# Kernel tuning notes

Hardware: AMD Instinct MI355X
Metric: run time of the kernel (lower is better)

Reference implementation:

```python
import jax, jax.numpy as jnp
import numpy as np

N = 20000
E = 640000
D = 128
NORM_FACTOR = 100.0
LN_EPS = 1e-5


def _layer_norm(x, g, b):
    mu = jnp.mean(x, axis=-1, keepdims=True)
    var = jnp.var(x, axis=-1, keepdims=True)
    return (x - mu) * jax.lax.rsqrt(var + LN_EPS) * g + b


def setup_inputs() -> dict:
    key = jax.random.key(0)
    ks = jax.random.split(key, 16)

    def lin(k, fan_in, shape):
        bound = 1.0 / np.sqrt(fan_in)
        return jax.random.uniform(k, shape, jnp.float32, -bound, bound)

    h = jax.random.normal(ks[0], (N, D), jnp.float32)
    distances = jax.random.uniform(ks[1], (E, 1), jnp.float32)
    edges = jax.random.randint(ks[2], (2, E), 0, N, jnp.int64)
    node_mask = jnp.ones((N, 1), jnp.float32)
    edge_mask = jnp.ones((E, 1), jnp.float32)

    return {
        "h": h, "distances": distances, "node_mask": node_mask, "edge_mask": edge_mask,
        # linear: in->out
        "lin_w": lin(ks[3], D, (D, D)), "lin_b": lin(ks[4], D, (D,)),
        # att_mlp: (2D+1)->2D -> 2D->D -> D->1
        "att_w1": lin(ks[5], 2 * D + 1, (2 * D, 2 * D + 1)), "att_b1": lin(ks[5], 2 * D + 1, (2 * D,)),
        "att_w2": lin(ks[6], 2 * D, (D, 2 * D)), "att_b2": lin(ks[6], 2 * D, (D,)),
        "att_w3": lin(ks[7], D, (1, D)), "att_b3": lin(ks[7], D, (1,)),
        # node_mlp: D->D, LN, SiLU, D->D
        "nm_w1": lin(ks[8], D, (D, D)), "nm_b1": lin(ks[8], D, (D,)),
        "nm_ln_g": jnp.ones((D,), jnp.float32), "nm_ln_b": jnp.zeros((D,), jnp.float32),
        "nm_w2": lin(ks[9], D, (D, D)), "nm_b2": lin(ks[9], D, (D,)),
        # final LayerNorm
        "ln_g": jnp.ones((D,), jnp.float32), "ln_b": jnp.zeros((D,), jnp.float32),
        "edges": edges,
    }


def reference(h, distances, node_mask, edge_mask,
              lin_w, lin_b, att_w1, att_b1, att_w2, att_b2, att_w3, att_b3,
              nm_w1, nm_b1, nm_ln_g, nm_ln_b, nm_w2, nm_b2, ln_g, ln_b, edges):
    x = h @ lin_w.T + lin_b                                  # [N, D]
    row, col = edges[0], edges[1]
    x_row = x[row]                                           # [E, D]
    x_col = x[col]                                           # [E, D]

    # DenseAtt
    d = distances * edge_mask
    x_cat = jnp.concatenate([x_row, x_col, d], axis=1)       # [E, 2D+1]
    a = jax.nn.silu(x_cat @ att_w1.T + att_b1)
    a = jax.nn.silu(a @ att_w2.T + att_b2)
    att = jax.nn.sigmoid(a @ att_w3.T + att_b3) * edge_mask  # [E, 1]

    agg = x_col * att                                        # [E, D]
    out = jax.ops.segment_sum(agg, row, num_segments=N) / NORM_FACTOR

    # node_mlp + residual
    o = out @ nm_w1.T + nm_b1
    o = jax.nn.silu(_layer_norm(o, nm_ln_g, nm_ln_b))
    o = o @ nm_w2.T + nm_b2
    hh = o + x

    hh = _layer_norm(hh, ln_g, ln_b)
    hh = jax.nn.silu(hh)                                     # act = SiLU
    return hh
```

## Files before the change

### kernel.cpp

```cpp
#include <hip/hip_runtime.h>
#include <hip/hip_bf16.h>

#define N_NODES 20000
#define E_EDGES 640000
#define DIM 128
#define CAP 96
#define EPB 64
#define NPB 8
#define XST 264

typedef __attribute__((ext_vector_type(8))) short bf16x8;
typedef __attribute__((ext_vector_type(4))) float f32x4;
typedef __attribute__((ext_vector_type(2))) float f32x2;
typedef __attribute__((ext_vector_type(4))) unsigned u32x4;

#define LOG2E 1.44269504f
__device__ __forceinline__ float fsilu(float x) {
    return x * __builtin_amdgcn_rcpf(1.f + __builtin_amdgcn_exp2f(-LOG2E * x));
}
__device__ __forceinline__ float fsig(float x) {
    return __builtin_amdgcn_rcpf(1.f + __builtin_amdgcn_exp2f(-LOG2E * x));
}
__device__ __forceinline__ f32x2 fsilu2(f32x2 v) {
    f32x2 m = v * (-LOG2E);
    f32x2 e; e.x = __builtin_amdgcn_exp2f(m.x); e.y = __builtin_amdgcn_exp2f(m.y);
    f32x2 den = e + 1.0f;
    f32x2 r; r.x = __builtin_amdgcn_rcpf(den.x); r.y = __builtin_amdgcn_rcpf(den.y);
    return v * r;
}

__device__ __forceinline__ unsigned short f2bf(float x) {
    union { float f; unsigned u; } v; v.f = x;
    unsigned r = (v.u + 0x7fffu + ((v.u >> 16) & 1u)) >> 16;
    return (unsigned short)r;
}
__device__ __forceinline__ float bf2f(unsigned short s) {
    union { unsigned u; float f; } v; v.u = ((unsigned)s) << 16;
    return v.f;
}
__device__ __forceinline__ unsigned pack_bf16(float lo, float hi) {
    union { float f; unsigned u; } a, b; a.f = lo; b.f = hi;
    unsigned ul = a.u + 0x8000u, uh = b.u + 0x8000u;
    return __builtin_amdgcn_perm(uh, ul, 0x07060302u);
}

#define PRE_PREP_BLOCKS 64
#define PRE_LIN_BLOCKS  625
#define PRE_ADJ_BLOCKS  2500
__global__ __launch_bounds__(256) void pre_kernel(
    const float* __restrict__ w1, const float* __restrict__ w2,
    unsigned short* __restrict__ w1b, float* __restrict__ w1p,
    unsigned short* __restrict__ w2b,
    const float* __restrict__ h, const float* __restrict__ lw,
    const float* __restrict__ lb, float* __restrict__ x,
    unsigned short* __restrict__ xb,
    const int* __restrict__ edges, int* __restrict__ cnt,
    int2* __restrict__ adj2, int E) {
    __shared__ float hs[32][128];
    int b = blockIdx.x;
    int t = threadIdx.x;

    if (b < PRE_PREP_BLOCKS) {
        int i = b * 256 + t;
        const int stride = PRE_PREP_BLOCKS * 256;
        for (int idx = i; idx < 256 * 256; idx += stride) {
            int o = idx >> 8, k = idx & 255;
            w1b[idx] = f2bf(w1[o * 257 + k]);
        }
        for (int idx = i; idx < 128 * 256; idx += stride) {
            int n2 = idx >> 8, p = idx & 255;
            int bb = p & ~31, off = p & 31;
            int ksrc = bb + (off >> 1) + ((off & 1) << 4);
            w2b[idx] = f2bf(w2[n2 * 256 + ksrc]);
        }
        for (int idx = i; idx < 256; idx += stride) {
            int bb = idx & ~31, off = idx & 31;
            int ksrc = bb + (off >> 1) + ((off & 1) << 4);
            w1p[idx] = w1[ksrc * 257 + 256];
        }
    } else if (b < PRE_PREP_BLOCKS + PRE_LIN_BLOCKS) {
        int nb = b - PRE_PREP_BLOCKS;
        int n0 = nb * 32;
        int ch = t & 127, g = t >> 7;
#pragma unroll
        for (int j = 0; j < 16; ++j) hs[g * 16 + j][ch] = h[(size_t)(n0 + g * 16 + j) * DIM + ch];
        __syncthreads();
        float acc[16];
#pragma unroll
        for (int j = 0; j < 16; ++j) acc[j] = 0.f;
        for (int kc = 0; kc < 128; kc += 4) {
            float4 wv = *(const float4*)&lw[(size_t)ch * DIM + kc];
#pragma unroll
            for (int j = 0; j < 16; ++j) {
                float4 hv = *(const float4*)&hs[g * 16 + j][kc];
                acc[j] += wv.x * hv.x + wv.y * hv.y + wv.z * hv.z + wv.w * hv.w;
            }
        }
        float bias = lb[ch];
#pragma unroll
        for (int j = 0; j < 16; ++j) {
            float v = acc[j] + bias;
            int n = n0 + g * 16 + j;
            x[(size_t)n * DIM + ch] = v;
            xb[(size_t)n * DIM + ch] = f2bf(v);
        }
    } else {
        int e = (b - PRE_PREP_BLOCKS - PRE_LIN_BLOCKS) * 256 + t;
        if (e < E) {
            int r = edges[e];
            int col = edges[E + e];
            int slot = atomicAdd(&cnt[r], 1);
            if (slot < CAP) { int2 v; v.x = e; v.y = col; adj2[(size_t)r * CAP + slot] = v; }
        }
    }
}

#define PRC_NPB 16
__global__ __launch_bounds__(256) void prc_kernel(
    const unsigned short* __restrict__ xb,
    const unsigned short* __restrict__ w1b,
    const float* __restrict__ b1,
    unsigned short* __restrict__ prb, unsigned short* __restrict__ pcb) {
    int n0 = blockIdx.x * PRC_NPB;
    int w = threadIdx.x >> 6, lane = threadIdx.x & 63;
    int lrow = lane & 15, quad = lane >> 4;

    bf16x8 a[4];
#pragma unroll
    for (int kk = 0; kk < 4; ++kk)
        a[kk] = *(const bf16x8*)&xb[(size_t)(n0 + lrow) * DIM + kk * 32 + quad * 8];

    f32x4 z = {0.f, 0.f, 0.f, 0.f};
#pragma unroll
    for (int i = 0; i < 8; ++i) {
        int gt = w * 8 + i;
        int half = gt >> 4;
        int obase = (gt & 15) * 16;
        f32x4 acc = z;
#pragma unroll
        for (int kk = 0; kk < 4; ++kk) {
            bf16x8 bfrag = *(const bf16x8*)&w1b[(size_t)(obase + lrow) * 256 + half * 128 + kk * 32 + quad * 8];
            acc = __builtin_amdgcn_mfma_f32_16x16x32_bf16(a[kk], bfrag, acc, 0, 0, 0);
        }
        int o = obase + lrow;
        if (half == 0) {
            float bias = b1[o];
#pragma unroll
            for (int r = 0; r < 4; ++r)
                prb[(size_t)(n0 + quad * 4 + r) * 256 + o] = f2bf(acc[r] + bias);
        } else {
#pragma unroll
            for (int r = 0; r < 4; ++r)
                pcb[(size_t)(n0 + quad * 4 + r) * 256 + o] = f2bf(acc[r]);
        }
    }
}

__global__ __launch_bounds__(512, 4) void edge_kernel(
    const unsigned short* __restrict__ prb, const unsigned short* __restrict__ pcb,
    const float* __restrict__ dist, const float* __restrict__ emask,
    const int* __restrict__ edges,
    const float* __restrict__ w1p,
    const unsigned short* __restrict__ w2b, const float* __restrict__ b2,
    const float* __restrict__ w3, const float* __restrict__ b3v,
    float* __restrict__ attv, int E) {
    __shared__ unsigned short buf[EPB * XST];
    __shared__ float part[8][EPB];
    __shared__ float w1ps[256];

    int tid = threadIdx.x;
    int eb = blockIdx.x * EPB;

    if (tid < 256) w1ps[tid] = w1p[tid];

    int ge = tid >> 3, cb = tid & 7;
    int e = eb + ge;
    int r = edges[e];
    int c2 = edges[E + e];
    float d = dist[e] * emask[e];
    const unsigned short* prow = prb + (size_t)r * 256 + cb * 32;
    const unsigned short* pcp  = pcb + (size_t)c2 * 256 + cb * 32;

    bf16x8 pA0 = *(const bf16x8*)&prow[0];
    bf16x8 pB0 = *(const bf16x8*)&prow[16];
    bf16x8 qA0 = *(const bf16x8*)&pcp[0];
    bf16x8 qB0 = *(const bf16x8*)&pcp[16];
    bf16x8 pA1 = *(const bf16x8*)&prow[8];
    bf16x8 pB1 = *(const bf16x8*)&prow[24];
    bf16x8 qA1 = *(const bf16x8*)&pcp[8];
    bf16x8 qB1 = *(const bf16x8*)&pcp[24];

    int wave = tid >> 6, lane = tid & 63;
    int lrow = lane & 15, quad = lane >> 4;
    int n2 = wave * 16 + lrow;
    float bias2 = b2[n2];
    float w3v = w3[n2];

    __syncthreads();

    {
        const float* wp = &w1ps[cb * 32];
        f32x2 d2 = {d, d};
        unsigned u[16];
#pragma unroll
        for (int l = 0; l < 8; ++l) {
            f32x2 p = {bf2f((unsigned short)pA0[l]), bf2f((unsigned short)pB0[l])};
            f32x2 q = {bf2f((unsigned short)qA0[l]), bf2f((unsigned short)qB0[l])};
            f32x2 wv2 = *(const f32x2*)&wp[2 * l];
            f32x2 sv = fsilu2(p + q + d2 * wv2);
            u[l] = pack_bf16(sv.x, sv.y);
        }
#pragma unroll
        for (int l = 0; l < 8; ++l) {
            f32x2 p = {bf2f((unsigned short)pA1[l]), bf2f((unsigned short)pB1[l])};
            f32x2 q = {bf2f((unsigned short)qA1[l]), bf2f((unsigned short)qB1[l])};
            f32x2 wv2 = *(const f32x2*)&wp[16 + 2 * l];
            f32x2 sv = fsilu2(p + q + d2 * wv2);
            u[8 + l] = pack_bf16(sv.x, sv.y);
        }
        u32x4* w4 = (u32x4*)&buf[ge * XST + cb * 32];
        u32x4 v0 = {u[0], u[1], u[2], u[3]};
        u32x4 v1 = {u[4], u[5], u[6], u[7]};
        u32x4 v2 = {u[8], u[9], u[10], u[11]};
        u32x4 v3 = {u[12], u[13], u[14], u[15]};
        w4[0] = v0; w4[1] = v1; w4[2] = v2; w4[3] = v3;
    }
    __syncthreads();

    f32x4 zz = {0.f, 0.f, 0.f, 0.f};
    f32x4 acc2[4];
#pragma unroll
    for (int mt = 0; mt < 4; ++mt) acc2[mt] = zz;

    for (int kk = 0; kk < 8; ++kk) {
        int ka = kk * 32 + quad * 8;
        bf16x8 bfrag = *(const bf16x8*)&w2b[(size_t)n2 * 256 + ka];
#pragma unroll
        for (int mt = 0; mt < 4; ++mt) {
            bf16x8 a = *(bf16x8*)&buf[(mt * 16 + lrow) * XST + ka];
            acc2[mt] = __builtin_amdgcn_mfma_f32_16x16x32_bf16(a, bfrag, acc2[mt], 0, 0, 0);
        }
    }

    float s[4][4];
#pragma unroll
    for (int mt = 0; mt < 4; ++mt)
#pragma unroll
        for (int r2 = 0; r2 < 4; ++r2)
            s[mt][r2] = fsilu(acc2[mt][r2] + bias2) * w3v;
#pragma unroll
    for (int off2 = 1; off2 < 16; off2 <<= 1) {
#pragma unroll
        for (int mt = 0; mt < 4; ++mt)
#pragma unroll
            for (int r2 = 0; r2 < 4; ++r2)
                s[mt][r2] += __shfl_xor(s[mt][r2], off2);
    }
    if (lrow == 0) {
#pragma unroll
        for (int mt = 0; mt < 4; ++mt)
#pragma unroll
            for (int r2 = 0; r2 < 4; ++r2)
                part[wave][mt * 16 + quad * 4 + r2] = s[mt][r2];
    }
    __syncthreads();

    if (tid < EPB) {
        float ssum = b3v[0];
#pragma unroll
        for (int w = 0; w < 8; ++w) ssum += part[w][tid];
        attv[eb + tid] = fsig(ssum) * emask[eb + tid];
    }
}

__global__ __launch_bounds__(256) void node_kernel(
    const float* __restrict__ attv, const int2* __restrict__ adj2,
    const int* __restrict__ cnt,
    const unsigned short* __restrict__ xb,
    const float* __restrict__ x,
    const float* __restrict__ w1, const float* __restrict__ bb1,
    const float* __restrict__ lng, const float* __restrict__ lnb,
    const float* __restrict__ w2, const float* __restrict__ bb2,
    const float* __restrict__ gF, const float* __restrict__ bF,
    float* __restrict__ out, int E) {
    __shared__ float atts[NPB][CAP];
    __shared__ int   cols[NPB][CAP];
    __shared__ float outv[NPB][128];
    __shared__ float bufs[NPB][128];
    __shared__ float mu_s[NPB], rs_s[NPB];
    __shared__ int cnts[NPB];

    int t = threadIdx.x;
    int n0 = blockIdx.x * NPB;

    if (t < NPB) { int c = cnt[n0 + t]; cnts[t] = c > CAP ? CAP : c; }
    __syncthreads();

    {
        int jg = t >> 5, l = t & 31;
        int c = cnts[jg];
        const int2* al = adj2 + (size_t)(n0 + jg) * CAP;
        for (int i = l; i < c; i += 32) {
            int2 v = al[i];
            atts[jg][i] = attv[v.x];
            cols[jg][i] = v.y;
        }
    }
    __syncthreads();

    int w = t >> 6, lane = t & 63;
    int islot = lane >> 4;
    int co = lane & 15;
#pragma unroll
    for (int jj = 0; jj < 2; ++jj) {
        int j = w * 2 + jj;
        int c = cnts[j];
        float acc[8];
#pragma unroll
        for (int k = 0; k < 8; ++k) acc[k] = 0.f;
        for (int base = 0; base < c; base += 8) {
            int i0 = base + islot, i1 = base + 4 + islot;
            bool k0 = i0 < c, k1 = i1 < c;
            int c0 = cols[j][k0 ? i0 : 0];
            int c1 = cols[j][k1 ? i1 : 0];
            float a0 = k0 ? atts[j][i0] : 0.f;
            float a1 = k1 ? atts[j][i1] : 0.f;
            bf16x8 q0 = *(const bf16x8*)&xb[(size_t)c0 * DIM + co * 8];
            bf16x8 q1 = *(const bf16x8*)&xb[(size_t)c1 * DIM + co * 8];
#pragma unroll
            for (int k = 0; k < 8; ++k) acc[k] += a0 * bf2f((unsigned short)q0[k]);
#pragma unroll
            for (int k = 0; k < 8; ++k) acc[k] += a1 * bf2f((unsigned short)q1[k]);
        }
#pragma unroll
        for (int k = 0; k < 8; ++k) {
            acc[k] += __shfl_xor(acc[k], 16);
            acc[k] += __shfl_xor(acc[k], 32);
        }
        if (islot == 0) {
            float4 v0 = {acc[0] * 0.01f, acc[1] * 0.01f, acc[2] * 0.01f, acc[3] * 0.01f};
            float4 v1 = {acc[4] * 0.01f, acc[5] * 0.01f, acc[6] * 0.01f, acc[7] * 0.01f};
            *(float4*)&outv[j][co * 8] = v0;
            *(float4*)&outv[j][co * 8 + 4] = v1;
        }
    }
    __syncthreads();

    int h = t >> 7, ch = t & 127;
    float xres[4];
#pragma unroll
    for (int jj = 0; jj < 4; ++jj)
        xres[jj] = x[(size_t)(n0 + h * 4 + jj) * DIM + ch];

    float a1[4] = {0, 0, 0, 0};
    for (int kc = 0; kc < 128; kc += 4) {
        float4 wv = *(const float4*)&w1[(size_t)ch * DIM + kc];
#pragma unroll
        for (int jj = 0; jj < 4; ++jj) {
            int j = h * 4 + jj;
            float4 ov = *(const float4*)&outv[j][kc];
            a1[jj] += wv.x * ov.x + wv.y * ov.y + wv.z * ov.z + wv.w * ov.w;
        }
    }
    float bias1 = bb1[ch];
#pragma unroll
    for (int jj = 0; jj < 4; ++jj) bufs[h * 4 + jj][ch] = a1[jj] + bias1;
    __syncthreads();

    {
        int j = t >> 5, l = t & 31;
        float s = 0.f, qq = 0.f;
#pragma unroll
        for (int i = 0; i < 4; ++i) { float v = bufs[j][l + 32 * i]; s += v; qq += v * v; }
#pragma unroll
        for (int off2 = 16; off2; off2 >>= 1) { s += __shfl_xor(s, off2); qq += __shfl_xor(qq, off2); }
        if (l == 0) {
            float mu = s * (1.f / 128.f);
            float var = qq * (1.f / 128.f) - mu * mu;
            mu_s[j] = mu; rs_s[j] = __builtin_amdgcn_rsqf(var + 1e-5f);
        }
    }
    __syncthreads();

    float g = lng[ch], bb = lnb[ch];
    float h2[4];
#pragma unroll
    for (int jj = 0; jj < 4; ++jj) {
        int j = h * 4 + jj;
        h2[jj] = fsilu((bufs[j][ch] - mu_s[j]) * rs_s[j] * g + bb);
    }
    __syncthreads();
#pragma unroll
    for (int jj = 0; jj < 4; ++jj) bufs[h * 4 + jj][ch] = h2[jj];
    __syncthreads();

    float a3[4] = {0, 0, 0, 0};
    for (int kc = 0; kc < 128; kc += 4) {
        float4 wv = *(const float4*)&w2[(size_t)ch * DIM + kc];
#pragma unroll
        for (int jj = 0; jj < 4; ++jj) {
            int j = h * 4 + jj;
            float4 bv = *(const float4*)&bufs[j][kc];
            a3[jj] += wv.x * bv.x + wv.y * bv.y + wv.z * bv.z + wv.w * bv.w;
        }
    }
    float bias2 = bb2[ch];
    float hh[4];
#pragma unroll
    for (int jj = 0; jj < 4; ++jj) hh[jj] = a3[jj] + bias2 + xres[jj];
    __syncthreads();
#pragma unroll
    for (int jj = 0; jj < 4; ++jj) bufs[h * 4 + jj][ch] = hh[jj];
    __syncthreads();

    {
        int j = t >> 5, l = t & 31;
        float s = 0.f, qq = 0.f;
#pragma unroll
        for (int i = 0; i < 4; ++i) { float v = bufs[j][l + 32 * i]; s += v; qq += v * v; }
#pragma unroll
        for (int off2 = 16; off2; off2 >>= 1) { s += __shfl_xor(s, off2); qq += __shfl_xor(qq, off2); }
        if (l == 0) {
            float mu = s * (1.f / 128.f);
            float var = qq * (1.f / 128.f) - mu * mu;
            mu_s[j] = mu; rs_s[j] = __builtin_amdgcn_rsqf(var + 1e-5f);
        }
    }
    __syncthreads();

    float gf = gF[ch], bf = bF[ch];
#pragma unroll
    for (int jj = 0; jj < 4; ++jj) {
        int j = h * 4 + jj;
        float y = (hh[jj] - mu_s[j]) * rs_s[j] * gf + bf;
        out[(size_t)(n0 + j) * DIM + ch] = fsilu(y);
    }
}

extern "C" void kernel_launch(void* const* d_in, const int* in_sizes, int n_in,
                              void* d_out, int out_size, void* d_ws, size_t ws_size,
                              hipStream_t stream) {
    const float* h         = (const float*)d_in[0];
    const float* distances = (const float*)d_in[1];
    const float* edge_mask = (const float*)d_in[3];
    const float* lin_w     = (const float*)d_in[4];
    const float* lin_b     = (const float*)d_in[5];
    const float* att_w1    = (const float*)d_in[6];
    const float* att_b1    = (const float*)d_in[7];
    const float* att_w2    = (const float*)d_in[8];
    const float* att_b2    = (const float*)d_in[9];
    const float* att_w3    = (const float*)d_in[10];
    const float* att_b3    = (const float*)d_in[11];
    const float* nm_w1     = (const float*)d_in[12];
    const float* nm_b1     = (const float*)d_in[13];
    const float* nm_ln_g   = (const float*)d_in[14];
    const float* nm_ln_b   = (const float*)d_in[15];
    const float* nm_w2     = (const float*)d_in[16];
    const float* nm_b2     = (const float*)d_in[17];
    const float* ln_g      = (const float*)d_in[18];
    const float* ln_b      = (const float*)d_in[19];
    const int*   edges     = (const int*)d_in[20];
    float* out = (float*)d_out;

    const int N = N_NODES, E = E_EDGES;

    char* ws = (char*)d_ws;
    float* x            = (float*)ws;            ws += (size_t)N * DIM * 4;
    unsigned short* xb  = (unsigned short*)ws;   ws += (size_t)N * DIM * 2;
    int* cnt            = (int*)ws;              ws += (size_t)N * 4;
    int2* adj2          = (int2*)ws;             ws += (size_t)N * CAP * 8;
    float* attv         = (float*)ws;            ws += (size_t)E * 4;
    unsigned short* w1b = (unsigned short*)ws;   ws += 256 * 256 * 2;
    float* w1p          = (float*)ws;            ws += 256 * 4;
    unsigned short* w2b = (unsigned short*)ws;   ws += 128 * 256 * 2;
    unsigned short* prb = (unsigned short*)ws;   ws += (size_t)N * 256 * 2;
    unsigned short* pcb = (unsigned short*)ws;   ws += (size_t)N * 256 * 2;

    hipMemsetAsync(cnt, 0, (size_t)N * 4, stream);

    pre_kernel<<<PRE_PREP_BLOCKS + PRE_LIN_BLOCKS + PRE_ADJ_BLOCKS, 256, 0, stream>>>(
        att_w1, att_w2, w1b, w1p, w2b,
        h, lin_w, lin_b, x, xb,
        edges, cnt, adj2, E);
    prc_kernel<<<N / PRC_NPB, 256, 0, stream>>>(xb, w1b, att_b1, prb, pcb);
    edge_kernel<<<E / EPB, 512, 0, stream>>>(prb, pcb, distances, edge_mask, edges,
                                             w1p, w2b, att_b2,
                                             att_w3, att_b3, attv, E);
    node_kernel<<<N / NPB, 256, 0, stream>>>(attv, adj2, cnt, xb, x,
                                             nm_w1, nm_b1, nm_ln_g, nm_ln_b,
                                             nm_w2, nm_b2, ln_g, ln_b, out, E);
}
```

Baseline: 410.1 us.

## Stage edge indices in LDS and rework node gather to per-lane channel pairs

The edge kernel now has 64 threads load edge indices, distances and masks into shared memory once per edge, rather than eight threads per edge loading the same values. Its gathers are split into two halves so fewer registers stay live at once. The node aggregation now gives each lane two channels and walks neighbours sequentially with 4-way unrolled independent accumulators. This drops the cross-lane shuffle reduction, at the cost of narrower 4-byte gathers per lane.

Result: faster. 400.2 us (-2.4%).

```diff
diff --git a/kernel.cpp b/kernel.cpp
--- a/kernel.cpp
+++ b/kernel.cpp
@@ -167,28 +167,21 @@
     __shared__ unsigned short buf[EPB * XST];
     __shared__ float part[8][EPB];
     __shared__ float w1ps[256];
+    __shared__ float dvals[EPB], emv[EPB];
+    __shared__ int ridx[EPB], cidx[EPB];
 
     int tid = threadIdx.x;
     int eb = blockIdx.x * EPB;
 
-    if (tid < 256) w1ps[tid] = w1p[tid];
-
-    int ge = tid >> 3, cb = tid & 7;
-    int e = eb + ge;
-    int r = edges[e];
-    int c2 = edges[E + e];
-    float d = dist[e] * emask[e];
-    const unsigned short* prow = prb + (size_t)r * 256 + cb * 32;
-    const unsigned short* pcp  = pcb + (size_t)c2 * 256 + cb * 32;
-
-    bf16x8 pA0 = *(const bf16x8*)&prow[0];
-    bf16x8 pB0 = *(const bf16x8*)&prow[16];
-    bf16x8 qA0 = *(const bf16x8*)&pcp[0];
-    bf16x8 qB0 = *(const bf16x8*)&pcp[16];
-    bf16x8 pA1 = *(const bf16x8*)&prow[8];
-    bf16x8 pB1 = *(const bf16x8*)&prow[24];
-    bf16x8 qA1 = *(const bf16x8*)&pcp[8];
-    bf16x8 qB1 = *(const bf16x8*)&pcp[24];
+    if (tid < EPB) {
+        int e = eb + tid;
+        ridx[tid] = edges[e];
+        cidx[tid] = edges[E + e];
+        float em = emask[e];
+        dvals[tid] = dist[e] * em;
+        emv[tid] = em;
+    }
+    if (tid >= 64 && tid < 320) w1ps[tid - 64] = w1p[tid - 64];
 
     int wave = tid >> 6, lane = tid & 63;
     int lrow = lane & 15, quad = lane >> 4;
@@ -199,21 +192,34 @@
     __syncthreads();
 
     {
+        int ge = tid >> 3, cb = tid & 7;
+        const unsigned short* prow = prb + (size_t)ridx[ge] * 256 + cb * 32;
+        const unsigned short* pcp  = pcb + (size_t)cidx[ge] * 256 + cb * 32;
+        float d = dvals[ge];
         const float* wp = &w1ps[cb * 32];
         f32x2 d2 = {d, d};
         unsigned u[16];
+
+        bf16x8 pA = *(const bf16x8*)&prow[0];
+        bf16x8 pB = *(const bf16x8*)&prow[16];
+        bf16x8 qA = *(const bf16x8*)&pcp[0];
+        bf16x8 qB = *(const bf16x8*)&pcp[16];
 #pragma unroll
         for (int l = 0; l < 8; ++l) {
-            f32x2 p = {bf2f((unsigned short)pA0[l]), bf2f((unsigned short)pB0[l])};
-            f32x2 q = {bf2f((unsigned short)qA0[l]), bf2f((unsigned short)qB0[l])};
+            f32x2 p = {bf2f((unsigned short)pA[l]), bf2f((unsigned short)pB[l])};
+            f32x2 q = {bf2f((unsigned short)qA[l]), bf2f((unsigned short)qB[l])};
             f32x2 wv2 = *(const f32x2*)&wp[2 * l];
             f32x2 sv = fsilu2(p + q + d2 * wv2);
             u[l] = pack_bf16(sv.x, sv.y);
         }
+        pA = *(const bf16x8*)&prow[8];
+        pB = *(const bf16x8*)&prow[24];
+        qA = *(const bf16x8*)&pcp[8];
+        qB = *(const bf16x8*)&pcp[24];
 #pragma unroll
         for (int l = 0; l < 8; ++l) {
-            f32x2 p = {bf2f((unsigned short)pA1[l]), bf2f((unsigned short)pB1[l])};
-            f32x2 q = {bf2f((unsigned short)qA1[l]), bf2f((unsigned short)qB1[l])};
+            f32x2 p = {bf2f((unsigned short)pA[l]), bf2f((unsigned short)pB[l])};
+            f32x2 q = {bf2f((unsigned short)qA[l]), bf2f((unsigned short)qB[l])};
             f32x2 wv2 = *(const f32x2*)&wp[16 + 2 * l];
             f32x2 sv = fsilu2(p + q + d2 * wv2);
             u[8 + l] = pack_bf16(sv.x, sv.y);
@@ -269,7 +275,7 @@
         float ssum = b3v[0];
 #pragma unroll
         for (int w = 0; w < 8; ++w) ssum += part[w][tid];
-        attv[eb + tid] = fsig(ssum) * emask[eb + tid];
+        attv[eb + tid] = fsig(ssum) * emv[tid];
     }
 }
 
@@ -309,40 +315,32 @@
     __syncthreads();
 
     int w = t >> 6, lane = t & 63;
-    int islot = lane >> 4;
-    int co = lane & 15;
 #pragma unroll
     for (int jj = 0; jj < 2; ++jj) {
         int j = w * 2 + jj;
         int c = cnts[j];
-        float acc[8];
-#pragma unroll
-        for (int k = 0; k < 8; ++k) acc[k] = 0.f;
-        for (int base = 0; base < c; base += 8) {
-            int i0 = base + islot, i1 = base + 4 + islot;
-            bool k0 = i0 < c, k1 = i1 < c;
-            int c0 = cols[j][k0 ? i0 : 0];
-            int c1 = cols[j][k1 ? i1 : 0];
-            float a0 = k0 ? atts[j][i0] : 0.f;
-            float a1 = k1 ? atts[j][i1] : 0.f;
-            bf16x8 q0 = *(const bf16x8*)&xb[(size_t)c0 * DIM + co * 8];
-            bf16x8 q1 = *(const bf16x8*)&xb[(size_t)c1 * DIM + co * 8];
-#pragma unroll
-            for (int k = 0; k < 8; ++k) acc[k] += a0 * bf2f((unsigned short)q0[k]);
-#pragma unroll
-            for (int k = 0; k < 8; ++k) acc[k] += a1 * bf2f((unsigned short)q1[k]);
-        }
-#pragma unroll
-        for (int k = 0; k < 8; ++k) {
-            acc[k] += __shfl_xor(acc[k], 16);
-            acc[k] += __shfl_xor(acc[k], 32);
-        }
-        if (islot == 0) {
-            float4 v0 = {acc[0] * 0.01f, acc[1] * 0.01f, acc[2] * 0.01f, acc[3] * 0.01f};
-            float4 v1 = {acc[4] * 0.01f, acc[5] * 0.01f, acc[6] * 0.01f, acc[7] * 0.01f};
-            *(float4*)&outv[j][co * 8] = v0;
-            *(float4*)&outv[j][co * 8 + 4] = v1;
-        }
+        float lo0 = 0.f, hi0 = 0.f, lo1 = 0.f, hi1 = 0.f;
+        float lo2 = 0.f, hi2 = 0.f, lo3 = 0.f, hi3 = 0.f;
+        int i = 0;
+        for (; i + 3 < c; i += 4) {
+            unsigned u0 = *(const unsigned*)&xb[(size_t)cols[j][i]     * DIM + lane * 2];
+            unsigned u1 = *(const unsigned*)&xb[(size_t)cols[j][i + 1] * DIM + lane * 2];
+            unsigned u2 = *(const unsigned*)&xb[(size_t)cols[j][i + 2] * DIM + lane * 2];
+            unsigned u3 = *(const unsigned*)&xb[(size_t)cols[j][i + 3] * DIM + lane * 2];
+            float w0 = atts[j][i], w1v = atts[j][i + 1], w2v = atts[j][i + 2], w3v = atts[j][i + 3];
+            lo0 += w0 * bf2f((unsigned short)(u0 & 0xffff)); hi0 += w0 * bf2f((unsigned short)(u0 >> 16));
+            lo1 += w1v * bf2f((unsigned short)(u1 & 0xffff)); hi1 += w1v * bf2f((unsigned short)(u1 >> 16));
+            lo2 += w2v * bf2f((unsigned short)(u2 & 0xffff)); hi2 += w2v * bf2f((unsigned short)(u2 >> 16));
+            lo3 += w3v * bf2f((unsigned short)(u3 & 0xffff)); hi3 += w3v * bf2f((unsigned short)(u3 >> 16));
+        }
+        for (; i < c; ++i) {
+            unsigned u0 = *(const unsigned*)&xb[(size_t)cols[j][i] * DIM + lane * 2];
+            float w0 = atts[j][i];
+            lo0 += w0 * bf2f((unsigned short)(u0 & 0xffff));
+            hi0 += w0 * bf2f((unsigned short)(u0 >> 16));
+        }
+        outv[j][lane * 2]     = ((lo0 + lo1) + (lo2 + lo3)) * 0.01f;
+        outv[j][lane * 2 + 1] = ((hi0 + hi1) + (hi2 + hi3)) * 0.01f;
     }
     __syncthreads();
 
```
